# Optimization experiments

Measured on AMD Instinct MI355X. Metric: run time of the kernel, lower is better.

Reference implementation:

```python
import jax, jax.numpy as jnp
import numpy as np

B, T, D = 2, 512, 1024
H = 16
DH = D // H          # 64 head dim
E = 8                # experts
K = 2                # top-k routing
F = 4 * D            # expert hidden dim


def _layernorm(x, s, b, eps=1e-5):
    mu = jnp.mean(x, axis=-1, keepdims=True)
    var = jnp.var(x, axis=-1, keepdims=True)
    return (x - mu) * jax.lax.rsqrt(var + eps) * s + b


def setup_inputs() -> dict:
    key = jax.random.key(0)
    ks = jax.random.split(key, 16)
    sd = 0.02
    return {
        "x": jax.random.normal(ks[0], (B, T, D), jnp.float32),
        "text_state": jax.random.normal(ks[1], (B, D), jnp.float32),
        "ln1_s": jnp.ones((D,), jnp.float32),
        "ln1_b": jnp.zeros((D,), jnp.float32),
        "w_qkv": jax.random.normal(ks[2], (D, 3 * D), jnp.float32) * sd,
        "b_qkv": jnp.zeros((3 * D,), jnp.float32),
        "w_o": jax.random.normal(ks[3], (D, D), jnp.float32) * sd,
        "b_o": jnp.zeros((D,), jnp.float32),
        "rel_bias": jax.random.normal(ks[4], (H, 2 * T - 1), jnp.float32) * sd,
        "ln2_s": jnp.ones((D,), jnp.float32),
        "ln2_b": jnp.zeros((D,), jnp.float32),
        "w_txt": jax.random.normal(ks[5], (D, D), jnp.float32) * sd,
        "b_txt": jnp.zeros((D,), jnp.float32),
        "w_r": jax.random.normal(ks[6], (D, E), jnp.float32) * sd,
        "b_r": jnp.zeros((E,), jnp.float32),
        "w1": jax.random.normal(ks[7], (E, D, F), jnp.float32) * sd,
        "b1": jnp.zeros((E, F), jnp.float32),
        "w2": jax.random.normal(ks[8], (E, F, D), jnp.float32) * sd,
        "b2": jnp.zeros((E, D), jnp.float32),
    }


def reference(x, text_state, ln1_s, ln1_b, w_qkv, b_qkv, w_o, b_o, rel_bias,
              ln2_s, ln2_b, w_txt, b_txt, w_r, b_r, w1, b1, w2, b2):
    # ---- temporal-bias multi-head self-attention (pre-LN, residual) ----
    h = _layernorm(x, ln1_s, ln1_b)
    qkv = (h @ w_qkv + b_qkv).reshape(B, T, 3, H, DH)
    q, k, v = qkv[:, :, 0], qkv[:, :, 1], qkv[:, :, 2]       # [B,T,H,DH]
    scores = jnp.einsum("bthd,bshd->bhts", q, k) / np.sqrt(DH).astype(np.float32)
    idx = jnp.arange(T)
    rel = idx[None, :] - idx[:, None] + (T - 1)              # [T,T] in [0, 2T-2]
    scores = scores + rel_bias[:, rel][None]                 # broadcast [1,H,T,T]
    attn = jax.nn.softmax(scores, axis=-1)
    ctx = jnp.einsum("bhts,bshd->bthd", attn, v).reshape(B, T, D)
    x = x + ctx @ w_o + b_o

    # ---- top-k MoE feed-forward with text-conditioned router ----
    h2 = _layernorm(x, ln2_s, ln2_b)
    router_in = h2 + (text_state @ w_txt + b_txt)[:, None, :]
    probs = jax.nn.softmax(router_in @ w_r + b_r, axis=-1)   # [B,T,E]
    topv, topi = jax.lax.top_k(probs, K)                     # [B,T,K]
    gates = topv / jnp.sum(topv, axis=-1, keepdims=True)
    gates_full = jnp.einsum("btk,btke->bte", gates, jax.nn.one_hot(topi, E, dtype=x.dtype))
    # dense grouped-expert compute, sparsely combined (same math as dispatch)
    hid = jax.nn.gelu(jnp.einsum("btd,edf->btef", h2, w1) + b1)      # [B,T,E,F]
    eout = jnp.einsum("btef,efd->bted", hid, w2) + b2                # [B,T,E,D]
    y = jnp.einsum("bte,bted->btd", gates_full, eout)
    x = x + y

    diag = jnp.mean(probs, axis=(0, 1))                      # expert load [E]
    return x, diag
```

## Files before the change

kernel.cpp:

```cpp
#include <hip/hip_runtime.h>
#include <hip/hip_bf16.h>
#include <math.h>

#define BB 2
#define TT 512
#define DD 1024
#define HH 16
#define DHH 64
#define EE 8
#define FF 4096
#define NTOK 1024
#define CAP 3072
#define SPL 2

typedef __attribute__((ext_vector_type(4))) float f32x4;
typedef __attribute__((ext_vector_type(8))) short short8;

__device__ __forceinline__ short f2b(float f) {
    __hip_bfloat16 h = __float2bfloat16(f);
    return *reinterpret_cast<short*>(&h);
}
__device__ __forceinline__ float b2f(short s) {
    __hip_bfloat16 h = *reinterpret_cast<__hip_bfloat16*>(&s);
    return __bfloat162float(h);
}

__device__ __forceinline__ void gload16(const short* g, short* l) {
    __builtin_amdgcn_global_load_lds((const __attribute__((address_space(1))) unsigned int*)g,
                                     (__attribute__((address_space(3))) unsigned int*)l,
                                     16, 0, 0);
}

__device__ __forceinline__ int seg_base(const int* counts, int e) {
    int a = 0;
    for (int i = 0; i < e; i++) a += (counts[i] + 127) & ~127;
    return a;
}

__device__ __forceinline__ void tc_tile(const float* __restrict__ src, short* __restrict__ dst,
                                        int K, int N, int k0, int n0, int tid, float* sm) {
    int nq = (tid & 15) * 4;
    int kq = (tid >> 4) * 4;
    float4 v[4];
    #pragma unroll
    for (int i = 0; i < 4; i++)
        v[i] = *(const float4*)&src[(size_t)(k0 + kq + i) * N + n0 + nq];
    #pragma unroll
    for (int j = 0; j < 4; j++) {
        float4 w;
        w.x = ((const float*)&v[0])[j];
        w.y = ((const float*)&v[1])[j];
        w.z = ((const float*)&v[2])[j];
        w.w = ((const float*)&v[3])[j];
        *(float4*)&sm[(nq + j) * 68 + kq] = w;
    }
    __syncthreads();
    int n = tid >> 2;
    int q = (tid & 3) * 16;
    short8 o0, o1;
    {
        float4 a = *(const float4*)&sm[n * 68 + q];
        float4 b = *(const float4*)&sm[n * 68 + q + 4];
        o0[0] = f2b(a.x); o0[1] = f2b(a.y); o0[2] = f2b(a.z); o0[3] = f2b(a.w);
        o0[4] = f2b(b.x); o0[5] = f2b(b.y); o0[6] = f2b(b.z); o0[7] = f2b(b.w);
    }
    {
        float4 a = *(const float4*)&sm[n * 68 + q + 8];
        float4 b = *(const float4*)&sm[n * 68 + q + 12];
        o1[0] = f2b(a.x); o1[1] = f2b(a.y); o1[2] = f2b(a.z); o1[3] = f2b(a.w);
        o1[4] = f2b(b.x); o1[5] = f2b(b.y); o1[6] = f2b(b.z); o1[7] = f2b(b.w);
    }
    *(short8*)&dst[(size_t)(n0 + n) * K + k0 + q]     = o0;
    *(short8*)&dst[(size_t)(n0 + n) * K + k0 + q + 8] = o1;
}

__device__ __forceinline__ void ln_row_bf16(const float* __restrict__ x, const float* __restrict__ s,
                                            const float* __restrict__ bsc, short* __restrict__ out,
                                            int row, int tid, float* sm) {
    const float* xr = x + (size_t)row * DD;
    float smv = 0.f, sq = 0.f;
    for (int i = tid; i < DD; i += 256) { float v = xr[i]; smv += v; sq += v * v; }
    #pragma unroll
    for (int o = 32; o; o >>= 1) { smv += __shfl_down(smv, o); sq += __shfl_down(sq, o); }
    if ((tid & 63) == 0) { sm[tid >> 6] = smv; sm[4 + (tid >> 6)] = sq; }
    __syncthreads();
    float tot = sm[0] + sm[1] + sm[2] + sm[3];
    float totq = sm[4] + sm[5] + sm[6] + sm[7];
    float mu = tot * (1.f / DD);
    float var = totq * (1.f / DD) - mu * mu;
    float inv = rsqrtf(var + 1e-5f);
    for (int i = tid; i < DD; i += 256)
        out[(size_t)row * DD + i] = f2b((xr[i] - mu) * inv * s[i] + bsc[i]);
}

__device__ __forceinline__ void txt_blk(const float* __restrict__ ts, const float* __restrict__ w,
                                        const float* __restrict__ bias, float* __restrict__ out,
                                        int b, int colblk, int tid, float* sm) {
    int col = colblk * 32 + (tid & 31);
    int dg = tid >> 5;
    float acc = 0.f;
    for (int d = dg * 128; d < dg * 128 + 128; d++)
        acc += ts[b * DD + d] * w[(size_t)d * DD + col];
    sm[dg * 32 + (tid & 31)] = acc;
    __syncthreads();
    if (tid < 32) {
        float s2 = 0.f;
        #pragma unroll
        for (int g = 0; g < 8; g++) s2 += sm[g * 32 + tid];
        out[b * DD + col] = s2 + bias[col];
    }
}

#define PREP_QKV   768
#define PREP_WO    1024
#define PREP_W1    9216
#define PREP_W2    17408
#define PREP_LN    18432
#define PREP_TXT   18496

__global__ __launch_bounds__(256) void prep_kernel(const float* __restrict__ w_qkv,
                                                   const float* __restrict__ w_o,
                                                   const float* __restrict__ w1,
                                                   const float* __restrict__ w2,
                                                   const float* __restrict__ x,
                                                   const float* __restrict__ ln1_s,
                                                   const float* __restrict__ ln1_b,
                                                   const float* __restrict__ ts,
                                                   const float* __restrict__ w_txt,
                                                   const float* __restrict__ b_txt,
                                                   short* __restrict__ wqkvT,
                                                   short* __restrict__ woT,
                                                   short* __restrict__ w1T,
                                                   short* __restrict__ w2T,
                                                   short* __restrict__ h1b,
                                                   float* __restrict__ txt) {
    __shared__ float sm[64 * 68];
    int idx = blockIdx.x, tid = threadIdx.x;
    if (idx < PREP_QKV) {
        int bx = idx % 48, by = idx / 48;
        tc_tile(w_qkv, wqkvT, DD, 3 * DD, by * 64, bx * 64, tid, sm);
    } else if (idx < PREP_WO) {
        int r = idx - PREP_QKV; int bx = r % 16, by = r / 16;
        tc_tile(w_o, woT, DD, DD, by * 64, bx * 64, tid, sm);
    } else if (idx < PREP_W1) {
        int r = idx - PREP_WO; int e = r >> 10; r &= 1023; int bx = r % 64, by = r / 64;
        tc_tile(w1 + (size_t)e * DD * FF, w1T + (size_t)e * FF * DD, DD, FF, by * 64, bx * 64, tid, sm);
    } else if (idx < PREP_W2) {
        int r = idx - PREP_W1; int e = r >> 10; r &= 1023; int bx = r % 16, by = r / 16;
        tc_tile(w2 + (size_t)e * FF * DD, w2T + (size_t)e * DD * FF, FF, DD, by * 64, bx * 64, tid, sm);
    } else if (idx < PREP_LN) {
        ln_row_bf16(x, ln1_s, ln1_b, h1b, idx - PREP_W2, tid, sm);
    } else {
        int r = idx - PREP_LN; int b = r >> 5, colblk = r & 31;
        txt_blk(ts, w_txt, b_txt, txt, b, colblk, tid, sm);
    }
}

__device__ __forceinline__ void gemm_loop128(const short* __restrict__ A,
                                             const short* __restrict__ B,
                                             int K, int lda, int ldb,
                                             short* As, short* Bs,
                                             f32x4 acc[4][4], int m0, int n0, int tid) {
    int wave = tid >> 6, lane = tid & 63;
    int wr = wave >> 1, wc = wave & 1;
    int lrow = lane & 15, lk = lane >> 4;
    int srow = lane >> 3;
    int sslot = (lane & 7) ^ srow;
    const short* Agb = A + (size_t)(m0 + srow) * lda + sslot * 8;
    const short* Bgb = B + (size_t)(n0 + srow) * ldb + sslot * 8;
    for (int k0 = 0; k0 < K; k0 += 64) {
        #pragma unroll
        for (int p = 0; p < 4; p++) {
            int rg = (wave * 4 + p) * 8;
            gload16(Agb + (size_t)rg * lda + k0, As + rg * 64);
            gload16(Bgb + (size_t)rg * ldb + k0, Bs + rg * 64);
        }
        __syncthreads();
        #pragma unroll
        for (int kk = 0; kk < 2; kk++) {
            int q = kk * 4 + lk;
            short8 a[4], b[4];
            #pragma unroll
            for (int i = 0; i < 4; i++) {
                int r = wr * 64 + i * 16 + lrow;
                uint4 v = ((const uint4*)As)[r * 8 + (q ^ (r & 7))];
                a[i] = *(short8*)&v;
            }
            #pragma unroll
            for (int j = 0; j < 4; j++) {
                int r = wc * 64 + j * 16 + lrow;
                uint4 v = ((const uint4*)Bs)[r * 8 + (q ^ (r & 7))];
                b[j] = *(short8*)&v;
            }
            #pragma unroll
            for (int i = 0; i < 4; i++)
                #pragma unroll
                for (int j = 0; j < 4; j++)
                    acc[i][j] = __builtin_amdgcn_mfma_f32_16x16x32_bf16(a[i], b[j], acc[i][j], 0, 0, 0);
        }
        __syncthreads();
    }
}

__device__ __forceinline__ void gemm_loop64(const short* __restrict__ A,
                                            const short* __restrict__ B,
                                            int K, int lda, int ldb,
                                            short* As, short* Bs,
                                            f32x4 acc[2][2], int m0, int n0, int tid) {
    int wave = tid >> 6, lane = tid & 63;
    int wr = wave >> 1, wc = wave & 1;
    int lrow = lane & 15, lk = lane >> 4;
    int sr = tid >> 3, ss = tid & 7;
    int sswz = (ss ^ (sr & 7)) * 8;
    const short* Ag0 = A + (size_t)(m0 + sr) * lda + sswz;
    const short* Ag1 = A + (size_t)(m0 + sr + 32) * lda + sswz;
    const short* Bg0 = B + (size_t)(n0 + sr) * ldb + sswz;
    const short* Bg1 = B + (size_t)(n0 + sr + 32) * ldb + sswz;
    short* lA0 = As + wave * 512;
    short* lA1 = As + 2048 + wave * 512;
    short* lB0 = Bs + wave * 512;
    short* lB1 = Bs + 2048 + wave * 512;
    int nt = K >> 6;
    gload16(Ag0, lA0); gload16(Ag1, lA1);
    gload16(Bg0, lB0); gload16(Bg1, lB1);
    __syncthreads();
    for (int t = 0; t < nt; ++t) {
        int h = (t & 1) * 4096;
        if (t + 1 < nt) {
            int k0 = (t + 1) << 6;
            int hn = 4096 - h;
            gload16(Ag0 + k0, lA0 + hn); gload16(Ag1 + k0, lA1 + hn);
            gload16(Bg0 + k0, lB0 + hn); gload16(Bg1 + k0, lB1 + hn);
        }
        const uint4* Asc = (const uint4*)(As + h);
        const uint4* Bsc = (const uint4*)(Bs + h);
        #pragma unroll
        for (int kk = 0; kk < 2; kk++) {
            int slot = kk * 4 + lk;
            short8 a[2], b[2];
            #pragma unroll
            for (int i = 0; i < 2; i++) {
                int row = wr * 32 + i * 16 + lrow;
                uint4 v = Asc[row * 8 + (slot ^ (row & 7))];
                a[i] = *(short8*)&v;
            }
            #pragma unroll
            for (int j = 0; j < 2; j++) {
                int row = wc * 32 + j * 16 + lrow;
                uint4 v = Bsc[row * 8 + (slot ^ (row & 7))];
                b[j] = *(short8*)&v;
            }
            #pragma unroll
            for (int i = 0; i < 2; i++)
                #pragma unroll
                for (int j = 0; j < 2; j++)
                    acc[i][j] = __builtin_amdgcn_mfma_f32_16x16x32_bf16(a[i], b[j], acc[i][j], 0, 0, 0);
        }
        __syncthreads();
    }
}

__device__ __forceinline__ void gemm_loop_w(const short* __restrict__ A,
                                            const short* __restrict__ B,
                                            int K, short* As, short* Bs,
                                            f32x4 acc[2][4], int m0, int n0, int tid) {
    int wave = tid >> 6, lane = tid & 63;
    int wr = wave >> 1, wc = wave & 1;
    int lrow = lane & 15, lk = lane >> 4;
    int sr = tid >> 3, ss = tid & 7;
    int sswz = (ss ^ (sr & 7)) * 8;
    const short* Ag0 = A + (size_t)(m0 + sr) * K + sswz;
    const short* Ag1 = A + (size_t)(m0 + sr + 32) * K + sswz;
    const short* Bg0 = B + (size_t)(n0 + sr) * K + sswz;
    const short* Bg1 = B + (size_t)(n0 + sr + 32) * K + sswz;
    const short* Bg2 = B + (size_t)(n0 + sr + 64) * K + sswz;
    const short* Bg3 = B + (size_t)(n0 + sr + 96) * K + sswz;
    short* lA0 = As + wave * 512;
    short* lA1 = As + 2048 + wave * 512;
    short* lB0 = Bs + wave * 512;
    short* lB1 = Bs + 2048 + wave * 512;
    short* lB2 = Bs + 4096 + wave * 512;
    short* lB3 = Bs + 6144 + wave * 512;
    int nt = K >> 6;
    gload16(Ag0, lA0); gload16(Ag1, lA1);
    gload16(Bg0, lB0); gload16(Bg1, lB1);
    gload16(Bg2, lB2); gload16(Bg3, lB3);
    __syncthreads();
    for (int t = 0; t < nt; ++t) {
        int hA = (t & 1) * 4096;
        int hB = (t & 1) * 8192;
        if (t + 1 < nt) {
            int k0 = (t + 1) << 6;
            int hnA = 4096 - hA, hnB = 8192 - hB;
            gload16(Ag0 + k0, lA0 + hnA); gload16(Ag1 + k0, lA1 + hnA);
            gload16(Bg0 + k0, lB0 + hnB); gload16(Bg1 + k0, lB1 + hnB);
            gload16(Bg2 + k0, lB2 + hnB); gload16(Bg3 + k0, lB3 + hnB);
        }
        const uint4* Asc = (const uint4*)(As + hA);
        const uint4* Bsc = (const uint4*)(Bs + hB);
        #pragma unroll
        for (int kk = 0; kk < 2; kk++) {
            int slot = kk * 4 + lk;
            short8 a[2], b[4];
            #pragma unroll
            for (int i = 0; i < 2; i++) {
                int row = wr * 32 + i * 16 + lrow;
                uint4 v = Asc[row * 8 + (slot ^ (row & 7))];
                a[i] = *(short8*)&v;
            }
            #pragma unroll
            for (int j = 0; j < 4; j++) {
                int row = wc * 64 + j * 16 + lrow;
                uint4 v = Bsc[row * 8 + (slot ^ (row & 7))];
                b[j] = *(short8*)&v;
            }
            #pragma unroll
            for (int i = 0; i < 2; i++)
                #pragma unroll
                for (int j = 0; j < 4; j++)
                    acc[i][j] = __builtin_amdgcn_mfma_f32_16x16x32_bf16(a[i], b[j], acc[i][j], 0, 0, 0);
        }
        __syncthreads();
    }
}

__global__ __launch_bounds__(256) void gemm64_res_mfma(const short* __restrict__ A,
                                                       const short* __restrict__ Bw,
                                                       const float* __restrict__ bias,
                                                       const float* __restrict__ res,
                                                       float* __restrict__ C,
                                                       int N, int K) {
    __shared__ short As[8192];
    __shared__ short Bs[8192];
    int tid = threadIdx.x;
    int m0 = blockIdx.y * 64, n0 = blockIdx.x * 64;
    f32x4 acc[2][2] = {};
    gemm_loop64(A, Bw, K, K, K, As, Bs, acc, m0, n0, tid);
    int wave = tid >> 6, lane = tid & 63;
    int wr = wave >> 1, wc = wave & 1;
    int lrow = lane & 15, lk = lane >> 4;
    #pragma unroll
    for (int i = 0; i < 2; i++) {
        #pragma unroll
        for (int j = 0; j < 2; j++) {
            int col = n0 + wc * 32 + j * 16 + lrow;
            float bv = bias[col];
            #pragma unroll
            for (int r = 0; r < 4; r++) {
                int row = m0 + wr * 32 + i * 16 + lk * 4 + r;
                C[(size_t)row * N + col] = acc[i][j][r] + bv + res[(size_t)row * N + col];
            }
        }
    }
}

__global__ __launch_bounds__(256) void qkv_mfma(const short* __restrict__ A,
                                                const short* __restrict__ Bw,
                                                const float* __restrict__ bias,
                                                short* __restrict__ Qb,
                                                short* __restrict__ Kb,
                                                short* __restrict__ VTb) {
    __shared__ short As[8192];
    __shared__ short Bs[16384];
    int tid = threadIdx.x;
    int m0 = blockIdx.y * 64, n0 = blockIdx.x * 128;
    f32x4 acc[2][4] = {};
    gemm_loop_w(A, Bw, DD, As, Bs, acc, m0, n0, tid);
    int wave = tid >> 6, lane = tid & 63;
    int wr = wave >> 1, wc = wave & 1;
    int lrow = lane & 15, lk = lane >> 4;
    #pragma unroll
    for (int i = 0; i < 2; i++) {
        #pragma unroll
        for (int j = 0; j < 4; j++) {
            int col = n0 + wc * 64 + j * 16 + lrow;
            int part = col >> 10;
            int rem = col & 1023;
            int h = rem >> 6, d = rem & 63;
            float bv = bias[col];
            #pragma unroll
            for (int r = 0; r < 4; r++) {
                int row = m0 + wr * 32 + i * 16 + lk * 4 + r;
                int b = row >> 9, t = row & (TT - 1);
                short val = f2b(acc[i][j][r] + bv);
                if (part == 0)      Qb[(((size_t)(b * HH + h)) * TT + t) * DHH + d] = val;
                else if (part == 1) Kb[(((size_t)(b * HH + h)) * TT + t) * DHH + d] = val;
                else                VTb[((size_t)(b * HH + h) * DHH + d) * TT + t] = val;
            }
        }
    }
}

__global__ __launch_bounds__(256) void scores_softmax(const short* __restrict__ Qb,
                                                      const short* __restrict__ Kb,
                                                      const float* __restrict__ rel_bias,
                                                      short* __restrict__ P) {
    __shared__ short As[64 * 64];
    __shared__ short Bs[128 * 64];
    __shared__ float red_m[64][2];
    __shared__ float red_s[64][2];
    int tid = threadIdx.x;
    int bh = blockIdx.y, h = bh & (HH - 1);
    int m0 = blockIdx.x * 64;
    const short* A  = Qb + (size_t)bh * TT * DHH;
    const short* Bk = Kb + (size_t)bh * TT * DHH;
    int wave = tid >> 6, lane = tid & 63;
    int wr = wave >> 1, wc = wave & 1;
    int l15 = lane & 15, lk = lane >> 4;
    int srow = lane >> 3;
    int sslot = (lane & 7) ^ srow;
    const short* Aq = A + (size_t)(m0 + srow) * DHH + sslot * 8;
    #pragma unroll
    for (int p2 = 0; p2 < 2; p2++) {
        int rg = (wave * 2 + p2) * 8;
        gload16(Aq + (size_t)rg * DHH, As + rg * 64);
    }
    f32x4 acc[4][2][4] = {};
    const short* Bb = Bk + (size_t)srow * DHH + sslot * 8;
    #pragma unroll
    for (int c = 0; c < 4; c++) {
        #pragma unroll
        for (int p = 0; p < 4; p++) {
            int rg = (wave * 4 + p) * 8;
            gload16(Bb + (size_t)(c * 128 + rg) * DHH, Bs + rg * 64);
        }
        __syncthreads();
        #pragma unroll
        for (int kk = 0; kk < 2; kk++) {
            int q = kk * 4 + lk;
            short8 a[2], b[4];
            #pragma unroll
            for (int i = 0; i < 2; i++) {
                int r = wr * 32 + i * 16 + l15;
                uint4 v = ((const uint4*)As)[r * 8 + (q ^ (r & 7))];
                a[i] = *(short8*)&v;
            }
            #pragma unroll
            for (int j = 0; j < 4; j++) {
                int r = wc * 64 + j * 16 + l15;
                uint4 v = ((const uint4*)Bs)[r * 8 + (q ^ (r & 7))];
                b[j] = *(short8*)&v;
            }
            #pragma unroll
            for (int i = 0; i < 2; i++)
                #pragma unroll
                for (int j = 0; j < 4; j++)
                    acc[c][i][j] = __builtin_amdgcn_mfma_f32_16x16x32_bf16(a[i], b[j], acc[c][i][j], 0, 0, 0);
        }
        __syncthreads();
    }
    int lk4 = lk * 4;
    const float* rb = rel_bias + h * (2 * TT - 1);
    #pragma unroll
    for (int i = 0; i < 2; i++) {
        #pragma unroll
        for (int r = 0; r < 4; r++) {
            int rowl = wr * 32 + i * 16 + lk4 + r;
            int bbase = 511 - m0 - rowl;
            float mx = -1e30f;
            #pragma unroll
            for (int c = 0; c < 4; c++) {
                #pragma unroll
                for (int j = 0; j < 4; j++) {
                    int col = c * 128 + wc * 64 + j * 16 + l15;
                    float v = acc[c][i][j][r] * 0.125f + rb[bbase + col];
                    acc[c][i][j][r] = v;
                    mx = fmaxf(mx, v);
                }
            }
            mx = fmaxf(mx, __shfl_xor(mx, 1));
            mx = fmaxf(mx, __shfl_xor(mx, 2));
            mx = fmaxf(mx, __shfl_xor(mx, 4));
            mx = fmaxf(mx, __shfl_xor(mx, 8));
            if (l15 == 0) red_m[rowl][wc] = mx;
        }
    }
    __syncthreads();
    #pragma unroll
    for (int i = 0; i < 2; i++) {
        #pragma unroll
        for (int r = 0; r < 4; r++) {
            int rowl = wr * 32 + i * 16 + lk4 + r;
            float m = fmaxf(red_m[rowl][0], red_m[rowl][1]);
            float s = 0.f;
            #pragma unroll
            for (int c = 0; c < 4; c++) {
                #pragma unroll
                for (int j = 0; j < 4; j++) {
                    float e = __expf(acc[c][i][j][r] - m);
                    acc[c][i][j][r] = e;
                    s += e;
                }
            }
            s += __shfl_xor(s, 1);
            s += __shfl_xor(s, 2);
            s += __shfl_xor(s, 4);
            s += __shfl_xor(s, 8);
            if (l15 == 0) red_s[rowl][wc] = s;
        }
    }
    __syncthreads();
    short* Pp = P + (size_t)bh * TT * TT;
    #pragma unroll
    for (int i = 0; i < 2; i++) {
        #pragma unroll
        for (int r = 0; r < 4; r++) {
            int rowl = wr * 32 + i * 16 + lk4 + r;
            float inv = 1.f / (red_s[rowl][0] + red_s[rowl][1]);
            #pragma unroll
            for (int c = 0; c < 4; c++) {
                #pragma unroll
                for (int j = 0; j < 4; j++) {
                    int col = c * 128 + wc * 64 + j * 16 + l15;
                    Pp[(size_t)(m0 + rowl) * TT + col] = f2b(acc[c][i][j][r] * inv);
                }
            }
        }
    }
}

__global__ __launch_bounds__(256) void pv_mfma(const short* __restrict__ P,
                                               const short* __restrict__ VTb,
                                               short* __restrict__ ctxb) {
    __shared__ short As[8192];
    __shared__ short Bs[8192];
    int tid = threadIdx.x;
    int bh = blockIdx.z;
    int h = bh & (HH - 1), b = bh >> 4;
    const short* A = P + (size_t)bh * TT * TT;
    const short* B = VTb + (size_t)bh * DHH * TT;
    int m0 = blockIdx.y * 64;
    f32x4 acc[2][2] = {};
    gemm_loop64(A, B, TT, TT, TT, As, Bs, acc, m0, 0, tid);
    int wave = tid >> 6, lane = tid & 63;
    int wr = wave >> 1, wc = wave & 1;
    int lrow = lane & 15, lk = lane >> 4;
    #pragma unroll
    for (int i = 0; i < 2; i++)
        #pragma unroll
        for (int j = 0; j < 2; j++) {
            int d = wc * 32 + j * 16 + lrow;
            #pragma unroll
            for (int r = 0; r < 4; r++) {
                int row = m0 + wr * 32 + i * 16 + lk * 4 + r;
                ctxb[((size_t)(b * TT + row)) * DD + h * DHH + d] = f2b(acc[i][j][r]);
            }
        }
}

__global__ __launch_bounds__(256) void ln_kernel_f32(const float* __restrict__ x,
                                                     const float* __restrict__ s,
                                                     const float* __restrict__ b,
                                                     float* __restrict__ outp) {
    int row = blockIdx.x;
    int tid = threadIdx.x;
    const float* xr = x + (size_t)row * DD;
    float sm = 0.f, sq = 0.f;
    for (int i = tid; i < DD; i += 256) { float v = xr[i]; sm += v; sq += v * v; }
    #pragma unroll
    for (int o = 32; o; o >>= 1) { sm += __shfl_down(sm, o); sq += __shfl_down(sq, o); }
    __shared__ float r1[4], r2[4];
    if ((tid & 63) == 0) { r1[tid >> 6] = sm; r2[tid >> 6] = sq; }
    __syncthreads();
    float tot = r1[0] + r1[1] + r1[2] + r1[3];
    float totq = r2[0] + r2[1] + r2[2] + r2[3];
    float mu = tot * (1.f / DD);
    float var = totq * (1.f / DD) - mu * mu;
    float inv = rsqrtf(var + 1e-5f);
    for (int i = tid; i < DD; i += 256)
        outp[(size_t)row * DD + i] = (xr[i] - mu) * inv * s[i] + b[i];
}

__global__ __launch_bounds__(256) void router_kernel(const float* __restrict__ h2,
                                                     const float* __restrict__ txt,
                                                     const float* __restrict__ w_r,
                                                     const float* __restrict__ b_r,
                                                     float* __restrict__ probs,
                                                     float* __restrict__ gates,
                                                     int* __restrict__ counts) {
    int row = blockIdx.x;
    int b = row >> 9;
    int tid = threadIdx.x;
    float acc[EE] = {};
    for (int d = tid; d < DD; d += 256) {
        float r = h2[(size_t)row * DD + d] + txt[b * DD + d];
        #pragma unroll
        for (int e = 0; e < EE; e++) acc[e] += r * w_r[d * EE + e];
    }
    #pragma unroll
    for (int e = 0; e < EE; e++)
        #pragma unroll
        for (int o = 32; o; o >>= 1) acc[e] += __shfl_down(acc[e], o);
    __shared__ float lds[4][EE];
    int lane = tid & 63, w = tid >> 6;
    if (lane == 0)
        for (int e = 0; e < EE; e++) lds[w][e] = acc[e];
    __syncthreads();
    if (tid == 0) {
        float lg[EE], p[EE];
        float mx = -1e30f;
        for (int e = 0; e < EE; e++) {
            lg[e] = lds[0][e] + lds[1][e] + lds[2][e] + lds[3][e] + b_r[e];
            mx = fmaxf(mx, lg[e]);
        }
        float sum = 0.f;
        for (int e = 0; e < EE; e++) { p[e] = expf(lg[e] - mx); sum += p[e]; }
        float invs = 1.f / sum;
        for (int e = 0; e < EE; e++) { p[e] *= invs; probs[row * EE + e] = p[e]; }
        int i1 = 0;
        for (int e = 1; e < EE; e++) if (p[e] > p[i1]) i1 = e;
        int i2 = (i1 == 0) ? 1 : 0;
        for (int e = 0; e < EE; e++) if (e != i1 && p[e] > p[i2]) i2 = e;
        float gs = p[i1] + p[i2];
        for (int e = 0; e < EE; e++) gates[row * EE + e] = 0.f;
        gates[row * EE + i1] = p[i1] / gs;
        gates[row * EE + i2] = p[i2] / gs;
        atomicAdd(&counts[i1], 1);
        atomicAdd(&counts[i2], 1);
    }
}

__global__ __launch_bounds__(256) void scatter_diag_kernel(const float* __restrict__ gates,
                                                           const float* __restrict__ probs,
                                                           const int* __restrict__ counts,
                                                           int* __restrict__ fill,
                                                           int* __restrict__ tok_pos,
                                                           float* __restrict__ pair_gate,
                                                           float* __restrict__ diag) {
    int blk = blockIdx.x;
    if (blk < 4) {
        int t = blk * 256 + threadIdx.x;
        int offs[EE];
        {
            int a = 0;
            #pragma unroll
            for (int e = 0; e < EE; e++) { offs[e] = a; a += (counts[e] + 127) & ~127; }
        }
        int slot = 0;
        for (int e = 0; e < EE; e++) {
            float g = gates[t * EE + e];
            if (g > 0.f) {
                int pos = offs[e] + atomicAdd(&fill[e], 1);
                tok_pos[t * 2 + slot] = pos;
                pair_gate[pos] = g;
                slot++;
            }
        }
    } else {
        int e = blk - 4;
        int tid = threadIdx.x;
        float s = 0.f;
        for (int t = tid; t < NTOK; t += 256) s += probs[t * EE + e];
        #pragma unroll
        for (int o = 32; o; o >>= 1) s += __shfl_down(s, o);
        __shared__ float red[4];
        if ((tid & 63) == 0) red[tid >> 6] = s;
        __syncthreads();
        if (tid == 0) diag[e] = (red[0] + red[1] + red[2] + red[3]) * (1.f / NTOK);
    }
}

__global__ __launch_bounds__(256) void gather_tokens(const float* __restrict__ h2,
                                                     const int* __restrict__ tok_pos,
                                                     short* __restrict__ Ag) {
    int i = blockIdx.x;
    int pos = tok_pos[i];
    int t = i >> 1;
    int d = threadIdx.x * 4;
    #pragma unroll
    for (int k = 0; k < 4; k++)
        Ag[(size_t)pos * DD + d + k] = f2b(h2[(size_t)t * DD + d + k]);
}

__global__ __launch_bounds__(256) void moe_gemm1_mfma(const short* __restrict__ Ag,
                                                      const short* __restrict__ W1t,
                                                      const float* __restrict__ b1,
                                                      const int* __restrict__ counts,
                                                      short* __restrict__ hid) {
    int e = blockIdx.y >> 4, tile = blockIdx.y & 15;
    int cnt = counts[e];
    int pcnt = (cnt + 127) & ~127;
    int row0 = tile * 128;
    if (row0 >= pcnt) return;
    int base = seg_base(counts, e);
    const short* A  = Ag + (size_t)base * DD;
    const short* Bw = W1t + (size_t)e * FF * DD;
    __shared__ short As[8192];
    __shared__ short Bs[8192];
    int tid = threadIdx.x;
    int n0 = blockIdx.x * 128;
    f32x4 acc[4][4] = {};
    gemm_loop128(A, Bw, DD, DD, DD, As, Bs, acc, row0, n0, tid);
    int wave = tid >> 6, lane = tid & 63;
    int wr = wave >> 1, wc = wave & 1;
    int lrow = lane & 15, lk = lane >> 4;
    #pragma unroll
    for (int i = 0; i < 4; i++) {
        #pragma unroll
        for (int j = 0; j < 4; j++) {
            int col = n0 + wc * 64 + j * 16 + lrow;
            float bv = b1[e * FF + col];
            #pragma unroll
            for (int r = 0; r < 4; r++) {
                int row = row0 + wr * 64 + i * 16 + lk * 4 + r;
                float v = acc[i][j][r] + bv;
                float u = 0.7978845608028654f * (v + 0.044715f * v * v * v);
                float g = 0.5f * v * (1.f + tanhf(u));
                hid[(size_t)(base + row) * FF + col] = f2b(g);
            }
        }
    }
}

__global__ __launch_bounds__(256) void moe_gemm2_mfma(const short* __restrict__ hid,
                                                      const short* __restrict__ W2t,
                                                      const float* __restrict__ b2,
                                                      const float* __restrict__ pair_gate,
                                                      const int* __restrict__ counts,
                                                      short* __restrict__ pair_part) {
    int s = blockIdx.z;
    int e = blockIdx.y >> 4, tile = blockIdx.y & 15;
    int cnt = counts[e];
    int pcnt = (cnt + 127) & ~127;
    int row0 = tile * 128;
    if (row0 >= pcnt) return;
    int base = seg_base(counts, e);
    const int KS = FF / SPL;
    const short* A  = hid + (size_t)base * FF + s * KS;
    const short* Bw = W2t + (size_t)e * DD * FF + s * KS;
    __shared__ short As[8192];
    __shared__ short Bs[8192];
    int tid = threadIdx.x;
    int n0 = blockIdx.x * 128;
    f32x4 acc[4][4] = {};
    gemm_loop128(A, Bw, KS, FF, FF, As, Bs, acc, row0, n0, tid);
    int wave = tid >> 6, lane = tid & 63;
    int wr = wave >> 1, wc = wave & 1;
    int lrow = lane & 15, lk = lane >> 4;
    #pragma unroll
    for (int i = 0; i < 4; i++) {
        #pragma unroll
        for (int j = 0; j < 4; j++) {
            int col = n0 + wc * 64 + j * 16 + lrow;
            float bv = (s == 0) ? b2[e * DD + col] : 0.f;
            #pragma unroll
            for (int r = 0; r < 4; r++) {
                int row = row0 + wr * 64 + i * 16 + lk * 4 + r;
                float g = pair_gate[base + row];
                pair_part[((size_t)s * CAP + base + row) * DD + col] = f2b(g * (acc[i][j][r] + bv));
            }
        }
    }
}

__global__ __launch_bounds__(256) void finaladd_kernel(float* __restrict__ out,
                                                       const short* __restrict__ pair_part,
                                                       const int* __restrict__ tok_pos) {
    int t = blockIdx.x;
    int d = threadIdx.x * 4;
    float4 a = *(const float4*)&out[(size_t)t * DD + d];
    #pragma unroll
    for (int sl = 0; sl < 2; sl++) {
        int pos = tok_pos[2 * t + sl];
        #pragma unroll
        for (int s = 0; s < SPL; s++) {
            short4 v = *(const short4*)&pair_part[((size_t)s * CAP + pos) * DD + d];
            a.x += b2f(v.x); a.y += b2f(v.y); a.z += b2f(v.z); a.w += b2f(v.w);
        }
    }
    *(float4*)&out[(size_t)t * DD + d] = a;
}

extern "C" void kernel_launch(void* const* d_in, const int* in_sizes, int n_in,
                              void* d_out, int out_size, void* d_ws, size_t ws_size,
                              hipStream_t stream) {
    const float* x          = (const float*)d_in[0];
    const float* text_state = (const float*)d_in[1];
    const float* ln1_s      = (const float*)d_in[2];
    const float* ln1_b      = (const float*)d_in[3];
    const float* w_qkv      = (const float*)d_in[4];
    const float* b_qkv      = (const float*)d_in[5];
    const float* w_o        = (const float*)d_in[6];
    const float* b_o        = (const float*)d_in[7];
    const float* rel_bias   = (const float*)d_in[8];
    const float* ln2_s      = (const float*)d_in[9];
    const float* ln2_b      = (const float*)d_in[10];
    const float* w_txt      = (const float*)d_in[11];
    const float* b_txt      = (const float*)d_in[12];
    const float* w_r        = (const float*)d_in[13];
    const float* b_r        = (const float*)d_in[14];
    const float* w1         = (const float*)d_in[15];
    const float* b1         = (const float*)d_in[16];
    const float* w2         = (const float*)d_in[17];
    const float* b2         = (const float*)d_in[18];

    float* out = (float*)d_out;

    char* p = (char*)d_ws;
    auto alloc = [&](size_t bytes) { char* r = p; p += (bytes + 255) & ~(size_t)255; return r; };
    short* h1b      = (short*)alloc((size_t)NTOK * DD * 2);
    short* Qb       = (short*)alloc((size_t)NTOK * DD * 2);
    short* Kb       = (short*)alloc((size_t)NTOK * DD * 2);
    short* VTb      = (short*)alloc((size_t)NTOK * DD * 2);
    short* Ag       = (short*)alloc((size_t)CAP * DD * 2);
    short* hid      = (short*)alloc((size_t)CAP * FF * 2);
    char*  region2  = alloc((size_t)BB * HH * TT * TT * 2);
    short* ctxb     = (short*)alloc((size_t)NTOK * DD * 2);
    float* h2       = (float*)alloc((size_t)NTOK * DD * 4);
    float* txt      = (float*)alloc((size_t)BB * DD * 4);
    float* probs    = (float*)alloc((size_t)NTOK * EE * 4);
    float* gates    = (float*)alloc((size_t)NTOK * EE * 4);
    float* pair_gate= (float*)alloc((size_t)CAP * 4);
    int*   iflags   = (int*)alloc(512);
    int*   counts   = iflags;
    int*   fill     = iflags + 64;
    int*   tok_pos  = (int*)alloc((size_t)NTOK * 2 * 4);
    short* wqkvT    = (short*)alloc((size_t)3 * DD * DD * 2);
    short* woT      = (short*)alloc((size_t)DD * DD * 2);
    short* w1T      = (short*)alloc((size_t)EE * FF * DD * 2);
    short* w2T      = (short*)alloc((size_t)EE * DD * FF * 2);

    short* P         = (short*)region2;
    short* pair_part = (short*)region2;

    prep_kernel<<<PREP_TXT, 256, 0, stream>>>(w_qkv, w_o, w1, w2, x, ln1_s, ln1_b,
                                              text_state, w_txt, b_txt,
                                              wqkvT, woT, w1T, w2T, h1b, txt);
    hipMemsetAsync(iflags, 0, 512, stream);
    qkv_mfma<<<dim3(3 * DD / 128, NTOK / 64), 256, 0, stream>>>(h1b, wqkvT, b_qkv, Qb, Kb, VTb);
    scores_softmax<<<dim3(TT / 64, BB * HH), 256, 0, stream>>>(Qb, Kb, rel_bias, P);
    pv_mfma<<<dim3(1, TT / 64, BB * HH), 256, 0, stream>>>(P, VTb, ctxb);
    gemm64_res_mfma<<<dim3(DD / 64, NTOK / 64), 256, 0, stream>>>(ctxb, woT, b_o, x, out, DD, DD);
    ln_kernel_f32<<<NTOK, 256, 0, stream>>>(out, ln2_s, ln2_b, h2);
    router_kernel<<<NTOK, 256, 0, stream>>>(h2, txt, w_r, b_r, probs, gates, counts);
    scatter_diag_kernel<<<12, 256, 0, stream>>>(gates, probs, counts, fill, tok_pos,
                                                pair_gate, out + (size_t)NTOK * DD);
    gather_tokens<<<NTOK * 2, 256, 0, stream>>>(h2, tok_pos, Ag);
    moe_gemm1_mfma<<<dim3(FF / 128, EE * 16), 256, 0, stream>>>(Ag, w1T, b1, counts, hid);
    moe_gemm2_mfma<<<dim3(DD / 128, EE * 16, SPL), 256, 0, stream>>>(hid, w2T, b2, pair_gate, counts, pair_part);
    finaladd_kernel<<<NTOK, 256, 0, stream>>>(out, pair_part, tok_pos);
}
```

Baseline: 350.5 us.

## Distribute MoE weight transpose blocks across attention kernels to overlap with compute

The large w1/w2 fp32-to-bf16 transpose work (16384 tile blocks) moves out of the prep kernel and is split across the qkv, scores, pv and output-projection kernels as extra trailing blocks. Those blocks run alongside the small attention grids, so the otherwise idle CUs do the memory-bound transpose instead of it being a serial front-loaded phase. Shared memory is unified into raw byte buffers and the grids are flattened to 1D to allow the extra blocks. The trade-off is that the transpose blocks compete for bandwidth and occupancy with the attention kernels, and the fixed split counts set how much each kernel takes.

```diff
diff --git a/kernel.cpp b/kernel.cpp
--- a/kernel.cpp
+++ b/kernel.cpp
@@ -73,6 +73,33 @@
     *(short8*)&dst[(size_t)(n0 + n) * K + k0 + q]     = o0;
     *(short8*)&dst[(size_t)(n0 + n) * K + k0 + q + 8] = o1;
 }
+
+__device__ __forceinline__ void moe_prep_block(int r, const float* __restrict__ w1,
+                                               const float* __restrict__ w2,
+                                               short* __restrict__ w1T,
+                                               short* __restrict__ w2T,
+                                               int tid, float* sm) {
+    if (r < 8192) {
+        int e = r >> 10, q = r & 1023;
+        int bx = q & 63, by = q >> 6;
+        tc_tile(w1 + (size_t)e * DD * FF, w1T + (size_t)e * FF * DD, DD, FF, by * 64, bx * 64, tid, sm);
+    } else {
+        r -= 8192;
+        int e = r >> 10, q = r & 1023;
+        int bx = q & 15, by = q >> 4;
+        tc_tile(w2 + (size_t)e * FF * DD, w2T + (size_t)e * DD * FF, FF, DD, by * 64, bx * 64, tid, sm);
+    }
+}
+
+#define NBAL        16384
+#define BAL_QKV_OFF 0
+#define BAL_QKV_N   5000
+#define BAL_SC_OFF  5000
+#define BAL_SC_N    5000
+#define BAL_PV_OFF  10000
+#define BAL_PV_N    3000
+#define BAL_WO_OFF  13000
+#define BAL_WO_N    3384
 
 __device__ __forceinline__ void ln_row_bf16(const float* __restrict__ x, const float* __restrict__ s,
                                             const float* __restrict__ bsc, short* __restrict__ out,
@@ -111,17 +138,13 @@
     }
 }
 
-#define PREP_QKV   768
-#define PREP_WO    1024
-#define PREP_W1    9216
-#define PREP_W2    17408
-#define PREP_LN    18432
-#define PREP_TXT   18496
+#define P1_QKV 768
+#define P1_WO  1024
+#define P1_LN  2048
+#define P1_TXT 2112
 
 __global__ __launch_bounds__(256) void prep_kernel(const float* __restrict__ w_qkv,
                                                    const float* __restrict__ w_o,
-                                                   const float* __restrict__ w1,
-                                                   const float* __restrict__ w2,
                                                    const float* __restrict__ x,
                                                    const float* __restrict__ ln1_s,
                                                    const float* __restrict__ ln1_b,
@@ -130,28 +153,20 @@
                                                    const float* __restrict__ b_txt,
                                                    short* __restrict__ wqkvT,
                                                    short* __restrict__ woT,
-                                                   short* __restrict__ w1T,
-                                                   short* __restrict__ w2T,
                                                    short* __restrict__ h1b,
                                                    float* __restrict__ txt) {
     __shared__ float sm[64 * 68];
     int idx = blockIdx.x, tid = threadIdx.x;
-    if (idx < PREP_QKV) {
+    if (idx < P1_QKV) {
         int bx = idx % 48, by = idx / 48;
         tc_tile(w_qkv, wqkvT, DD, 3 * DD, by * 64, bx * 64, tid, sm);
-    } else if (idx < PREP_WO) {
-        int r = idx - PREP_QKV; int bx = r % 16, by = r / 16;
+    } else if (idx < P1_WO) {
+        int r = idx - P1_QKV; int bx = r % 16, by = r / 16;
         tc_tile(w_o, woT, DD, DD, by * 64, bx * 64, tid, sm);
-    } else if (idx < PREP_W1) {
-        int r = idx - PREP_WO; int e = r >> 10; r &= 1023; int bx = r % 64, by = r / 64;
-        tc_tile(w1 + (size_t)e * DD * FF, w1T + (size_t)e * FF * DD, DD, FF, by * 64, bx * 64, tid, sm);
-    } else if (idx < PREP_W2) {
-        int r = idx - PREP_W1; int e = r >> 10; r &= 1023; int bx = r % 16, by = r / 16;
-        tc_tile(w2 + (size_t)e * FF * DD, w2T + (size_t)e * DD * FF, FF, DD, by * 64, bx * 64, tid, sm);
-    } else if (idx < PREP_LN) {
-        ln_row_bf16(x, ln1_s, ln1_b, h1b, idx - PREP_W2, tid, sm);
+    } else if (idx < P1_LN) {
+        ln_row_bf16(x, ln1_s, ln1_b, h1b, idx - P1_WO, tid, sm);
     } else {
-        int r = idx - PREP_LN; int b = r >> 5, colblk = r & 31;
+        int r = idx - P1_LN; int b = r >> 5, colblk = r & 31;
         txt_blk(ts, w_txt, b_txt, txt, b, colblk, tid, sm);
     }
 }
@@ -329,11 +344,21 @@
                                                        const float* __restrict__ bias,
                                                        const float* __restrict__ res,
                                                        float* __restrict__ C,
-                                                       int N, int K) {
-    __shared__ short As[8192];
-    __shared__ short Bs[8192];
+                                                       int N, int K,
+                                                       const float* __restrict__ w1,
+                                                       const float* __restrict__ w2,
+                                                       short* __restrict__ w1T,
+                                                       short* __restrict__ w2T) {
+    __shared__ __align__(16) char smraw[32768];
     int tid = threadIdx.x;
-    int m0 = blockIdx.y * 64, n0 = blockIdx.x * 64;
+    int idx = blockIdx.x;
+    if (idx >= 256) {
+        moe_prep_block(BAL_WO_OFF + idx - 256, w1, w2, w1T, w2T, tid, (float*)smraw);
+        return;
+    }
+    short* As = (short*)smraw;
+    short* Bs = (short*)(smraw + 16384);
+    int n0 = (idx & 15) * 64, m0 = (idx >> 4) * 64;
     f32x4 acc[2][2] = {};
     gemm_loop64(A, Bw, K, K, K, As, Bs, acc, m0, n0, tid);
     int wave = tid >> 6, lane = tid & 63;
@@ -359,11 +384,21 @@
                                                 const float* __restrict__ bias,
                                                 short* __restrict__ Qb,
                                                 short* __restrict__ Kb,
-                                                short* __restrict__ VTb) {
-    __shared__ short As[8192];
-    __shared__ short Bs[16384];
+                                                short* __restrict__ VTb,
+                                                const float* __restrict__ w1,
+                                                const float* __restrict__ w2,
+                                                short* __restrict__ w1T,
+                                                short* __restrict__ w2T) {
+    __shared__ __align__(16) char smraw[49152];
     int tid = threadIdx.x;
-    int m0 = blockIdx.y * 64, n0 = blockIdx.x * 128;
+    int idx = blockIdx.x;
+    if (idx >= 384) {
+        moe_prep_block(BAL_QKV_OFF + idx - 384, w1, w2, w1T, w2T, tid, (float*)smraw);
+        return;
+    }
+    short* As = (short*)smraw;
+    short* Bs = (short*)(smraw + 16384);
+    int m0 = (idx / 24) * 64, n0 = (idx % 24) * 128;
     f32x4 acc[2][4] = {};
     gemm_loop_w(A, Bw, DD, As, Bs, acc, m0, n0, tid);
     int wave = tid >> 6, lane = tid & 63;
@@ -394,14 +429,24 @@
 __global__ __launch_bounds__(256) void scores_softmax(const short* __restrict__ Qb,
                                                       const short* __restrict__ Kb,
                                                       const float* __restrict__ rel_bias,
-                                                      short* __restrict__ P) {
-    __shared__ short As[64 * 64];
-    __shared__ short Bs[128 * 64];
-    __shared__ float red_m[64][2];
-    __shared__ float red_s[64][2];
+                                                      short* __restrict__ P,
+                                                      const float* __restrict__ w1,
+                                                      const float* __restrict__ w2,
+                                                      short* __restrict__ w1T,
+                                                      short* __restrict__ w2T) {
+    __shared__ __align__(16) char smraw[25600];
     int tid = threadIdx.x;
-    int bh = blockIdx.y, h = bh & (HH - 1);
-    int m0 = blockIdx.x * 64;
+    int idx = blockIdx.x;
+    if (idx >= 256) {
+        moe_prep_block(BAL_SC_OFF + idx - 256, w1, w2, w1T, w2T, tid, (float*)smraw);
+        return;
+    }
+    short* As = (short*)smraw;
+    short* Bs = (short*)(smraw + 8192);
+    float (*red_m)[2] = (float(*)[2])(smraw + 24576);
+    float (*red_s)[2] = (float(*)[2])(smraw + 25088);
+    int bh = idx / 8, h = bh & (HH - 1);
+    int m0 = (idx & 7) * 64;
     const short* A  = Qb + (size_t)bh * TT * DHH;
     const short* Bk = Kb + (size_t)bh * TT * DHH;
     int wave = tid >> 6, lane = tid & 63;
@@ -521,15 +566,25 @@
 
 __global__ __launch_bounds__(256) void pv_mfma(const short* __restrict__ P,
                                                const short* __restrict__ VTb,
-                                               short* __restrict__ ctxb) {
-    __shared__ short As[8192];
-    __shared__ short Bs[8192];
+                                               short* __restrict__ ctxb,
+                                               const float* __restrict__ w1,
+                                               const float* __restrict__ w2,
+                                               short* __restrict__ w1T,
+                                               short* __restrict__ w2T) {
+    __shared__ __align__(16) char smraw[32768];
     int tid = threadIdx.x;
-    int bh = blockIdx.z;
+    int idx = blockIdx.x;
+    if (idx >= 256) {
+        moe_prep_block(BAL_PV_OFF + idx - 256, w1, w2, w1T, w2T, tid, (float*)smraw);
+        return;
+    }
+    short* As = (short*)smraw;
+    short* Bs = (short*)(smraw + 16384);
+    int bh = idx / 8;
     int h = bh & (HH - 1), b = bh >> 4;
     const short* A = P + (size_t)bh * TT * TT;
     const short* B = VTb + (size_t)bh * DHH * TT;
-    int m0 = blockIdx.y * 64;
+    int m0 = (idx & 7) * 64;
     f32x4 acc[2][2] = {};
     gemm_loop64(A, B, TT, TT, TT, As, Bs, acc, m0, 0, tid);
     int wave = tid >> 6, lane = tid & 63;
@@ -823,14 +878,17 @@
     short* P         = (short*)region2;
     short* pair_part = (short*)region2;
 
-    prep_kernel<<<PREP_TXT, 256, 0, stream>>>(w_qkv, w_o, w1, w2, x, ln1_s, ln1_b,
-                                              text_state, w_txt, b_txt,
-                                              wqkvT, woT, w1T, w2T, h1b, txt);
+    prep_kernel<<<P1_TXT, 256, 0, stream>>>(w_qkv, w_o, x, ln1_s, ln1_b,
+                                            text_state, w_txt, b_txt,
+                                            wqkvT, woT, h1b, txt);
     hipMemsetAsync(iflags, 0, 512, stream);
-    qkv_mfma<<<dim3(3 * DD / 128, NTOK / 64), 256, 0, stream>>>(h1b, wqkvT, b_qkv, Qb, Kb, VTb);
-    scores_softmax<<<dim3(TT / 64, BB * HH), 256, 0, stream>>>(Qb, Kb, rel_bias, P);
-    pv_mfma<<<dim3(1, TT / 64, BB * HH), 256, 0, stream>>>(P, VTb, ctxb);
-    gemm64_res_mfma<<<dim3(DD / 64, NTOK / 64), 256, 0, stream>>>(ctxb, woT, b_o, x, out, DD, DD);
+    qkv_mfma<<<384 + BAL_QKV_N, 256, 0, stream>>>(h1b, wqkvT, b_qkv, Qb, Kb, VTb,
+                                                  w1, w2, w1T, w2T);
+    scores_softmax<<<256 + BAL_SC_N, 256, 0, stream>>>(Qb, Kb, rel_bias, P,
+                                                       w1, w2, w1T, w2T);
+    pv_mfma<<<256 + BAL_PV_N, 256, 0, stream>>>(P, VTb, ctxb, w1, w2, w1T, w2T);
+    gemm64_res_mfma<<<256 + BAL_WO_N, 256, 0, stream>>>(ctxb, woT, b_o, x, out, DD, DD,
+                                                        w1, w2, w1T, w2T);
     ln_kernel_f32<<<NTOK, 256, 0, stream>>>(out, ln2_s, ln2_b, h2);
     router_kernel<<<NTOK, 256, 0, stream>>>(h2, txt, w_r, b_r, probs, gates, counts);
     scatter_diag_kernel<<<12, 256, 0, stream>>>(gates, probs, counts, fill, tok_pos,
```

Measured after the change: 339.6 us. 1.03x faster.

## Convert expert weights to bf16 on the fly inside MoE GEMM loads

Applied to the files above, without the earlier changes.

Removes the prep-kernel pass that transposed and cast all expert weights w1 and w2 to bf16. The MoE GEMMs now read the fp32 weights directly, convert them to bf16 while staging into a padded, swizzled shared-memory tile, and transpose them in registers. This avoids writing and re-reading the bf16 copies and shrinks the prep grid. In exchange, each active GEMM tile loads fp32 weights (twice the bytes) and pays conversion cost in the inner loop, with uncoalesced-ish shared-memory stores.

```diff
diff --git a/kernel.cpp b/kernel.cpp
--- a/kernel.cpp
+++ b/kernel.cpp
@@ -111,17 +111,13 @@
     }
 }
 
-#define PREP_QKV   768
-#define PREP_WO    1024
-#define PREP_W1    9216
-#define PREP_W2    17408
-#define PREP_LN    18432
-#define PREP_TXT   18496
+#define P1_QKV 768
+#define P1_WO  1024
+#define P1_LN  2048
+#define P1_TXT 2112
 
 __global__ __launch_bounds__(256) void prep_kernel(const float* __restrict__ w_qkv,
                                                    const float* __restrict__ w_o,
-                                                   const float* __restrict__ w1,
-                                                   const float* __restrict__ w2,
                                                    const float* __restrict__ x,
                                                    const float* __restrict__ ln1_s,
                                                    const float* __restrict__ ln1_b,
@@ -130,50 +126,64 @@
                                                    const float* __restrict__ b_txt,
                                                    short* __restrict__ wqkvT,
                                                    short* __restrict__ woT,
-                                                   short* __restrict__ w1T,
-                                                   short* __restrict__ w2T,
                                                    short* __restrict__ h1b,
                                                    float* __restrict__ txt) {
     __shared__ float sm[64 * 68];
     int idx = blockIdx.x, tid = threadIdx.x;
-    if (idx < PREP_QKV) {
+    if (idx < P1_QKV) {
         int bx = idx % 48, by = idx / 48;
         tc_tile(w_qkv, wqkvT, DD, 3 * DD, by * 64, bx * 64, tid, sm);
-    } else if (idx < PREP_WO) {
-        int r = idx - PREP_QKV; int bx = r % 16, by = r / 16;
+    } else if (idx < P1_WO) {
+        int r = idx - P1_QKV; int bx = r % 16, by = r / 16;
         tc_tile(w_o, woT, DD, DD, by * 64, bx * 64, tid, sm);
-    } else if (idx < PREP_W1) {
-        int r = idx - PREP_WO; int e = r >> 10; r &= 1023; int bx = r % 64, by = r / 64;
-        tc_tile(w1 + (size_t)e * DD * FF, w1T + (size_t)e * FF * DD, DD, FF, by * 64, bx * 64, tid, sm);
-    } else if (idx < PREP_W2) {
-        int r = idx - PREP_W1; int e = r >> 10; r &= 1023; int bx = r % 16, by = r / 16;
-        tc_tile(w2 + (size_t)e * FF * DD, w2T + (size_t)e * DD * FF, FF, DD, by * 64, bx * 64, tid, sm);
-    } else if (idx < PREP_LN) {
-        ln_row_bf16(x, ln1_s, ln1_b, h1b, idx - PREP_W2, tid, sm);
+    } else if (idx < P1_LN) {
+        ln_row_bf16(x, ln1_s, ln1_b, h1b, idx - P1_WO, tid, sm);
     } else {
-        int r = idx - PREP_LN; int b = r >> 5, colblk = r & 31;
+        int r = idx - P1_LN; int b = r >> 5, colblk = r & 31;
         txt_blk(ts, w_txt, b_txt, txt, b, colblk, tid, sm);
     }
 }
 
-__device__ __forceinline__ void gemm_loop128(const short* __restrict__ A,
-                                             const short* __restrict__ B,
-                                             int K, int lda, int ldb,
-                                             short* As, short* Bs,
-                                             f32x4 acc[4][4], int m0, int n0, int tid) {
+#define BPITCH 144
+__device__ __forceinline__ void gemm_loop128_f32B(const short* __restrict__ A,
+                                                  const float* __restrict__ Bg,
+                                                  int K, int lda, int ldbn,
+                                                  short* As, char* Bs,
+                                                  f32x4 acc[4][4], int m0, int n0, int tid) {
     int wave = tid >> 6, lane = tid & 63;
     int wr = wave >> 1, wc = wave & 1;
     int lrow = lane & 15, lk = lane >> 4;
     int srow = lane >> 3;
     int sslot = (lane & 7) ^ srow;
     const short* Agb = A + (size_t)(m0 + srow) * lda + sslot * 8;
-    const short* Bgb = B + (size_t)(n0 + srow) * ldb + sslot * 8;
+    int nq = tid & 31;
+    int kq0 = tid >> 5;
     for (int k0 = 0; k0 < K; k0 += 64) {
         #pragma unroll
         for (int p = 0; p < 4; p++) {
             int rg = (wave * 4 + p) * 8;
             gload16(Agb + (size_t)rg * lda + k0, As + rg * 64);
-            gload16(Bgb + (size_t)rg * ldb + k0, Bs + rg * 64);
+        }
+        #pragma unroll
+        for (int h = 0; h < 2; h++) {
+            int kq = kq0 + h * 8;
+            const float* src = Bg + (size_t)(k0 + kq * 4) * ldbn + n0 + nq * 4;
+            float4 v0 = *(const float4*)(src);
+            float4 v1 = *(const float4*)(src + ldbn);
+            float4 v2 = *(const float4*)(src + 2 * (size_t)ldbn);
+            float4 v3 = *(const float4*)(src + 3 * (size_t)ldbn);
+            int slot = kq >> 1;
+            int half = (kq & 1) * 8;
+            #pragma unroll
+            for (int j = 0; j < 4; j++) {
+                int r = nq * 4 + j;
+                short4 o;
+                o.x = f2b(((const float*)&v0)[j]);
+                o.y = f2b(((const float*)&v1)[j]);
+                o.z = f2b(((const float*)&v2)[j]);
+                o.w = f2b(((const float*)&v3)[j]);
+                *(short4*)(Bs + r * BPITCH + ((slot ^ (r & 7)) * 16) + half) = o;
+            }
         }
         __syncthreads();
         #pragma unroll
@@ -189,7 +199,7 @@
             #pragma unroll
             for (int j = 0; j < 4; j++) {
                 int r = wc * 64 + j * 16 + lrow;
-                uint4 v = ((const uint4*)Bs)[r * 8 + (q ^ (r & 7))];
+                uint4 v = *(const uint4*)(Bs + r * BPITCH + ((q ^ (r & 7)) * 16));
                 b[j] = *(short8*)&v;
             }
             #pragma unroll
@@ -673,7 +683,7 @@
 }
 
 __global__ __launch_bounds__(256) void moe_gemm1_mfma(const short* __restrict__ Ag,
-                                                      const short* __restrict__ W1t,
+                                                      const float* __restrict__ W1,
                                                       const float* __restrict__ b1,
                                                       const int* __restrict__ counts,
                                                       short* __restrict__ hid) {
@@ -684,13 +694,13 @@
     if (row0 >= pcnt) return;
     int base = seg_base(counts, e);
     const short* A  = Ag + (size_t)base * DD;
-    const short* Bw = W1t + (size_t)e * FF * DD;
+    const float* Bg = W1 + (size_t)e * DD * FF;
     __shared__ short As[8192];
-    __shared__ short Bs[8192];
+    __shared__ __align__(16) char Bs[128 * BPITCH];
     int tid = threadIdx.x;
     int n0 = blockIdx.x * 128;
     f32x4 acc[4][4] = {};
-    gemm_loop128(A, Bw, DD, DD, DD, As, Bs, acc, row0, n0, tid);
+    gemm_loop128_f32B(A, Bg, DD, DD, FF, As, Bs, acc, row0, n0, tid);
     int wave = tid >> 6, lane = tid & 63;
     int wr = wave >> 1, wc = wave & 1;
     int lrow = lane & 15, lk = lane >> 4;
@@ -713,7 +723,7 @@
 }
 
 __global__ __launch_bounds__(256) void moe_gemm2_mfma(const short* __restrict__ hid,
-                                                      const short* __restrict__ W2t,
+                                                      const float* __restrict__ W2,
                                                       const float* __restrict__ b2,
                                                       const float* __restrict__ pair_gate,
                                                       const int* __restrict__ counts,
@@ -727,13 +737,13 @@
     int base = seg_base(counts, e);
     const int KS = FF / SPL;
     const short* A  = hid + (size_t)base * FF + s * KS;
-    const short* Bw = W2t + (size_t)e * DD * FF + s * KS;
+    const float* Bg = W2 + (size_t)e * FF * DD + (size_t)s * KS * DD;
     __shared__ short As[8192];
-    __shared__ short Bs[8192];
+    __shared__ __align__(16) char Bs[128 * BPITCH];
     int tid = threadIdx.x;
     int n0 = blockIdx.x * 128;
     f32x4 acc[4][4] = {};
-    gemm_loop128(A, Bw, KS, FF, FF, As, Bs, acc, row0, n0, tid);
+    gemm_loop128_f32B(A, Bg, KS, FF, DD, As, Bs, acc, row0, n0, tid);
     int wave = tid >> 6, lane = tid & 63;
     int wr = wave >> 1, wc = wave & 1;
     int lrow = lane & 15, lk = lane >> 4;
@@ -817,15 +827,13 @@
     int*   tok_pos  = (int*)alloc((size_t)NTOK * 2 * 4);
     short* wqkvT    = (short*)alloc((size_t)3 * DD * DD * 2);
     short* woT      = (short*)alloc((size_t)DD * DD * 2);
-    short* w1T      = (short*)alloc((size_t)EE * FF * DD * 2);
-    short* w2T      = (short*)alloc((size_t)EE * DD * FF * 2);
 
     short* P         = (short*)region2;
     short* pair_part = (short*)region2;
 
-    prep_kernel<<<PREP_TXT, 256, 0, stream>>>(w_qkv, w_o, w1, w2, x, ln1_s, ln1_b,
-                                              text_state, w_txt, b_txt,
-                                              wqkvT, woT, w1T, w2T, h1b, txt);
+    prep_kernel<<<P1_TXT, 256, 0, stream>>>(w_qkv, w_o, x, ln1_s, ln1_b,
+                                            text_state, w_txt, b_txt,
+                                            wqkvT, woT, h1b, txt);
     hipMemsetAsync(iflags, 0, 512, stream);
     qkv_mfma<<<dim3(3 * DD / 128, NTOK / 64), 256, 0, stream>>>(h1b, wqkvT, b_qkv, Qb, Kb, VTb);
     scores_softmax<<<dim3(TT / 64, BB * HH), 256, 0, stream>>>(Qb, Kb, rel_bias, P);
@@ -836,7 +844,7 @@
     scatter_diag_kernel<<<12, 256, 0, stream>>>(gates, probs, counts, fill, tok_pos,
                                                 pair_gate, out + (size_t)NTOK * DD);
     gather_tokens<<<NTOK * 2, 256, 0, stream>>>(h2, tok_pos, Ag);
-    moe_gemm1_mfma<<<dim3(FF / 128, EE * 16), 256, 0, stream>>>(Ag, w1T, b1, counts, hid);
-    moe_gemm2_mfma<<<dim3(DD / 128, EE * 16, SPL), 256, 0, stream>>>(hid, w2T, b2, pair_gate, counts, pair_part);
+    moe_gemm1_mfma<<<dim3(FF / 128, EE * 16), 256, 0, stream>>>(Ag, w1, b1, counts, hid);
+    moe_gemm2_mfma<<<dim3(DD / 128, EE * 16, SPL), 256, 0, stream>>>(hid, w2, b2, pair_gate, counts, pair_part);
     finaladd_kernel<<<NTOK, 256, 0, stream>>>(out, pair_part, tok_pos);
 }
```

Result: slower. 407.6 us (+16.3%).
